# Optimization experiments

Hardware: AMD Instinct MI355X
Metric: run time of the kernel (lower is better)

Reference implementation:

```python
import jax, jax.numpy as jnp
import numpy as np

D_IN = 1024
D_OUT = 1024
N_HEADS = 16
HEAD_DIM = D_IN // N_HEADS      # 64
HEAD_DIM_V = D_OUT // N_HEADS   # 64


def setup_inputs() -> dict:
    key = jax.random.key(0)
    ks = jax.random.split(key, 7)
    s = 0.02
    x = jax.random.normal(ks[0], (4, 2048, D_IN), dtype=jnp.float32)
    Wq = jax.random.normal(ks[1], (D_IN, D_IN), dtype=jnp.float32) * s
    bq = jnp.zeros((D_IN,), dtype=jnp.float32)
    Wk = jax.random.normal(ks[2], (D_IN, D_IN), dtype=jnp.float32) * s
    bk = jnp.zeros((D_IN,), dtype=jnp.float32)
    Wv = jax.random.normal(ks[3], (D_IN, D_OUT), dtype=jnp.float32) * s
    bv = jnp.zeros((D_OUT,), dtype=jnp.float32)
    return {"x": x, "Wq": Wq, "bq": bq, "Wk": Wk, "bk": bk, "Wv": Wv, "bv": bv}


def reference(x, Wq, bq, Wk, bk, Wv, bv):
    B, S, _ = x.shape
    scale = jnp.sqrt(jnp.asarray(HEAD_DIM, dtype=jnp.float32))
    # projections -> [B, S, H, Dh] -> [B, H, S, Dh]
    q = (x @ Wq + bq).reshape(B, S, N_HEADS, HEAD_DIM).transpose(0, 2, 1, 3)
    k = (x @ Wk + bk).reshape(B, S, N_HEADS, HEAD_DIM).transpose(0, 2, 1, 3)
    v = (x @ Wv + bv).reshape(B, S, N_HEADS, HEAD_DIM_V).transpose(0, 2, 1, 3)
    # [B, H, S, S] attention scores (naive full materialization, as in source)
    scores = jnp.einsum("bhsd,bhtd->bhst", q, k) / scale
    weights = jax.nn.softmax(scores, axis=-1)
    out = jnp.einsum("bhst,bhtd->bhsd", weights, v)
    # [B, H, S, Dv] -> [B, S, H*Dv]  (out_projection NOT applied in source forward)
    return out.transpose(0, 2, 1, 3).reshape(B, S, N_HEADS * HEAD_DIM_V)
```

## Files before the change

### kernel.cpp

```cpp
#include <hip/hip_runtime.h>

#define B_  4
#define S_  2048
#define D_  1024
#define H_  16
#define DH_ 64
#define M_  (B_ * S_)

typedef __attribute__((ext_vector_type(8))) short short8;
typedef __attribute__((ext_vector_type(4))) float floatx4;

__device__ __forceinline__ float bf2f(unsigned short u) {
    union { unsigned int i; float f; } v; v.i = ((unsigned int)u) << 16; return v.f;
}
__device__ __forceinline__ unsigned short f2bf(float f) {
    union { float f; unsigned int i; } v; v.f = f;
    unsigned int r = v.i + 0x7fffu + ((v.i >> 16) & 1u);
    return (unsigned short)(r >> 16);
}
__device__ __forceinline__ unsigned int pk_trunc(float a, float b) {
    return (__float_as_uint(a) >> 16) | (__float_as_uint(b) & 0xffff0000u);
}

typedef const __attribute__((address_space(1))) unsigned int* gas_ptr;
typedef __attribute__((address_space(3))) unsigned int* las_ptr;
__device__ __forceinline__ void async_cp16(const void* g, void* l) {
    __builtin_amdgcn_global_load_lds((gas_ptr)g, (las_ptr)l, 16, 0, 0);
}

__global__ __launch_bounds__(256) void cast_x_kernel(
    const float* __restrict__ x, unsigned short* __restrict__ Ax)
{
    int i4 = blockIdx.x * 256 + threadIdx.x;
    float4 v = reinterpret_cast<const float4*>(x)[i4];
    ushort4 o;
    o.x = f2bf(v.x); o.y = f2bf(v.y); o.z = f2bf(v.z); o.w = f2bf(v.w);
    reinterpret_cast<ushort4*>(Ax)[i4] = o;
}

__global__ __launch_bounds__(256) void cast_w_T_kernel(
    const float* __restrict__ W, unsigned short* __restrict__ Wt)
{
    __shared__ unsigned short T[64][72];
    const int t = threadIdx.x;
    const int k0 = blockIdx.x * 64, n0 = blockIdx.y * 64;

    #pragma unroll
    for (int p = 0; p < 4; ++p) {
        int kr = p * 16 + (t >> 4);
        int nc = (t & 15) * 4;
        float4 v = *reinterpret_cast<const float4*>(W + (size_t)(k0 + kr) * D_ + n0 + nc);
        T[nc + 0][kr] = f2bf(v.x);
        T[nc + 1][kr] = f2bf(v.y);
        T[nc + 2][kr] = f2bf(v.z);
        T[nc + 3][kr] = f2bf(v.w);
    }
    __syncthreads();

    const int nl = t >> 2, kc = (t & 3) * 16;
    size_t base = (size_t)(n0 + nl) * D_ + k0 + kc;
    *reinterpret_cast<short8*>(Wt + base)     = *reinterpret_cast<const short8*>(&T[nl][kc]);
    *reinterpret_cast<short8*>(Wt + base + 8) = *reinterpret_cast<const short8*>(&T[nl][kc + 8]);
}

__global__ __launch_bounds__(256) void gemm_qkv_mfma(
    const unsigned short* __restrict__ Ax,
    const unsigned short* __restrict__ Wtq,
    const unsigned short* __restrict__ Wtk,
    const unsigned short* __restrict__ Wtv,
    const float* __restrict__ bq, const float* __restrict__ bk,
    const float* __restrict__ bv,
    unsigned short* __restrict__ Q, unsigned short* __restrict__ K,
    unsigned short* __restrict__ Vtg)
{
    __shared__ unsigned short As[128 * 32];
    __shared__ unsigned short Bs[128 * 32];

    const int tid = threadIdx.x;
    const int lane = tid & 63;
    const int w = tid >> 6;
    const int wm = (w >> 1) * 64, wn = (w & 1) * 64;
    const int l15 = lane & 15, quad = lane >> 4;

    const int hw   = blockIdx.x;
    const int xcd  = hw & 7;
    const int slot = hw >> 3;
    const int gcol = slot >> 3;
    const int mi   = slot & 7;
    const int m0   = (xcd * 8 + mi) * 128;
    const int n0   = (gcol & 7) * 128;
    const int mat  = gcol >> 3;

    const unsigned short* Wt = mat == 0 ? Wtq : (mat == 1 ? Wtk : Wtv);
    const float* bias        = mat == 0 ? bq  : (mat == 1 ? bk  : bv);

    const int arow = tid >> 2;
    const int acol = (tid & 3) * 8;

    floatx4 acc[4][4] = {};

    for (int kb = 0; kb < 32; ++kb) {
        int cb = kb * 32;
        __syncthreads();
        async_cp16(Ax + (size_t)(m0 + arow) * D_ + cb + acol,      As + arow * 32 + acol);
        async_cp16(Ax + (size_t)(m0 + 64 + arow) * D_ + cb + acol, As + (64 + arow) * 32 + acol);
        async_cp16(Wt + (size_t)(n0 + arow) * D_ + cb + acol,      Bs + arow * 32 + acol);
        async_cp16(Wt + (size_t)(n0 + 64 + arow) * D_ + cb + acol, Bs + (64 + arow) * 32 + acol);
        __syncthreads();

        short8 af[4], bf[4];
        #pragma unroll
        for (int i = 0; i < 4; ++i)
            af[i] = *reinterpret_cast<const short8*>(As + (wm + i * 16 + l15) * 32 + quad * 8);
        #pragma unroll
        for (int j = 0; j < 4; ++j)
            bf[j] = *reinterpret_cast<const short8*>(Bs + (wn + j * 16 + l15) * 32 + quad * 8);
        #pragma unroll
        for (int i = 0; i < 4; ++i)
            #pragma unroll
            for (int j = 0; j < 4; ++j)
                acc[i][j] = __builtin_amdgcn_mfma_f32_16x16x32_bf16(af[i], bf[j], acc[i][j], 0, 0, 0);
    }

    float bb[4];
    #pragma unroll
    for (int j = 0; j < 4; ++j) bb[j] = bias[n0 + wn + j * 16 + l15];

    if (mat == 2) {
        const int b = m0 >> 11;
        #pragma unroll
        for (int i = 0; i < 4; ++i) {
            int srow = (m0 & 2047) + wm + i * 16 + quad * 4;
            #pragma unroll
            for (int j = 0; j < 4; ++j) {
                int col = n0 + wn + j * 16 + l15;
                ushort4 o;
                o.x = f2bf(acc[i][j][0] + bb[j]);
                o.y = f2bf(acc[i][j][1] + bb[j]);
                o.z = f2bf(acc[i][j][2] + bb[j]);
                o.w = f2bf(acc[i][j][3] + bb[j]);
                *reinterpret_cast<ushort4*>(Vtg + (size_t)(b * 1024 + col) * S_ + srow) = o;
            }
        }
    } else {
        unsigned short* C = (mat == 0) ? Q : K;
        const float sc = (mat == 0) ? 0.125f : 1.0f;
        #pragma unroll
        for (int i = 0; i < 4; ++i)
            #pragma unroll
            for (int r = 0; r < 4; ++r) {
                int row = m0 + wm + i * 16 + quad * 4 + r;
                #pragma unroll
                for (int j = 0; j < 4; ++j)
                    C[(size_t)row * D_ + n0 + wn + j * 16 + l15] = f2bf((acc[i][j][r] + bb[j]) * sc);
            }
    }
}

#define KT_   64
#define PITCH 72

__global__ __launch_bounds__(256, 4) void attn_mfma(
    const unsigned short* __restrict__ Qg,
    const unsigned short* __restrict__ Kg,
    const unsigned short* __restrict__ Vtg,
    float* __restrict__ out)
{
    __shared__ unsigned short Ks[KT_ * PITCH];
    __shared__ unsigned short Vt[DH_ * PITCH];

    const int tid  = threadIdx.x;
    const int wq   = tid >> 6;
    const int lane = tid & 63;
    const int l15  = lane & 15;
    const int quad = lane >> 4;

    const int id  = blockIdx.x;
    const int bh  = (id & 7) * 8 + ((id >> 3) & 7);
    const int qt  = id >> 6;
    const int b   = bh >> 4;
    const int colbase = (bh & 15) * DH_;
    const int rowQ0 = b * S_ + qt * 128;

    short8 qf[2][2];
    #pragma unroll
    for (int g = 0; g < 2; ++g) {
        int qrow = rowQ0 + wq * 32 + g * 16 + l15;
        qf[g][0] = *reinterpret_cast<const short8*>(Qg + (size_t)qrow * D_ + colbase + quad * 8);
        qf[g][1] = *reinterpret_cast<const short8*>(Qg + (size_t)qrow * D_ + colbase + 32 + quad * 8);
    }

    floatx4 Oacc[2][4] = {};
    float lsum[2] = {0.f, 0.f};

    const int srow = tid >> 3;
    const int sc8  = (tid & 7) * 8;
    const int vc  = sc8 >> 4;
    const int vqk = (sc8 >> 2) & 3;
    const int vk0 = ((vc & 1) << 2) + ((vc >> 1) << 5) + (vqk << 3);

    const unsigned short* Kbase = Kg + (size_t)(b * S_) * D_ + colbase;
    const unsigned short* Vbase = Vtg + (size_t)(bh * 64) * S_;

    short8 kpre[2], vpre[2];
    #pragma unroll
    for (int p = 0; p < 2; ++p) {
        kpre[p] = *reinterpret_cast<const short8*>(Kbase + (size_t)(p * 32 + srow) * D_ + sc8);
        vpre[p] = *reinterpret_cast<const short8*>(Vbase + (size_t)(p * 32 + srow) * S_ + sc8);
    }

    for (int kt = 0; kt < S_ / KT_; ++kt) {
        __syncthreads();
        #pragma unroll
        for (int p = 0; p < 2; ++p) {
            *reinterpret_cast<short8*>(&Ks[(p * 32 + srow) * PITCH + sc8]) = kpre[p];
            uint4 u = __builtin_bit_cast(uint4, vpre[p]);
            uint2 lo, hi;
            lo.x = u.x; lo.y = u.y; hi.x = u.z; hi.y = u.w;
            *reinterpret_cast<uint2*>(&Vt[(p * 32 + srow) * PITCH + vk0])     = lo;
            *reinterpret_cast<uint2*>(&Vt[(p * 32 + srow) * PITCH + vk0 + 8]) = hi;
        }
        if (kt + 1 < S_ / KT_) {
            int off = (kt + 1) * KT_;
            #pragma unroll
            for (int p = 0; p < 2; ++p) {
                kpre[p] = *reinterpret_cast<const short8*>(Kbase + (size_t)(off + p * 32 + srow) * D_ + sc8);
                vpre[p] = *reinterpret_cast<const short8*>(Vbase + (size_t)(p * 32 + srow) * S_ + off + sc8);
            }
        }
        __syncthreads();

        #pragma unroll
        for (int half = 0; half < 2; ++half) {
            floatx4 s_[2][2];
            #pragma unroll
            for (int ci = 0; ci < 2; ++ci) {
                int c = half * 2 + ci;
                short8 kf0 = *reinterpret_cast<const short8*>(&Ks[(c * 16 + l15) * PITCH + quad * 8]);
                short8 kf1 = *reinterpret_cast<const short8*>(&Ks[(c * 16 + l15) * PITCH + 32 + quad * 8]);
                #pragma unroll
                for (int g = 0; g < 2; ++g) {
                    floatx4 a = {0.f, 0.f, 0.f, 0.f};
                    a = __builtin_amdgcn_mfma_f32_16x16x32_bf16(kf0, qf[g][0], a, 0, 0, 0);
                    a = __builtin_amdgcn_mfma_f32_16x16x32_bf16(kf1, qf[g][1], a, 0, 0, 0);
                    s_[g][ci] = a;
                }
            }
            short8 pa[2];
            #pragma unroll
            for (int g = 0; g < 2; ++g) {
                float p00 = __expf(s_[g][0][0]), p01 = __expf(s_[g][0][1]);
                float p02 = __expf(s_[g][0][2]), p03 = __expf(s_[g][0][3]);
                float p10 = __expf(s_[g][1][0]), p11 = __expf(s_[g][1][1]);
                float p12 = __expf(s_[g][1][2]), p13 = __expf(s_[g][1][3]);
                lsum[g] += (p00 + p01) + (p02 + p03) + (p10 + p11) + (p12 + p13);
                uint4 pu;
                pu.x = pk_trunc(p00, p01);
                pu.y = pk_trunc(p02, p03);
                pu.z = pk_trunc(p10, p11);
                pu.w = pk_trunc(p12, p13);
                pa[g] = __builtin_bit_cast(short8, pu);
            }
            #pragma unroll
            for (int d = 0; d < 4; ++d) {
                short8 vf = *reinterpret_cast<const short8*>(
                    &Vt[(d * 16 + l15) * PITCH + half * 32 + quad * 8]);
                #pragma unroll
                for (int g = 0; g < 2; ++g)
                    Oacc[g][d] = __builtin_amdgcn_mfma_f32_16x16x32_bf16(pa[g], vf, Oacc[g][d], 0, 0, 0);
            }
        }
    }

    #pragma unroll
    for (int g = 0; g < 2; ++g) {
        float lred = lsum[g];
        lred += __shfl_xor(lred, 16);
        lred += __shfl_xor(lred, 32);
        float inv[4];
        #pragma unroll
        for (int r = 0; r < 4; ++r)
            inv[r] = 1.f / __shfl(lred, quad * 4 + r);
        int orow = rowQ0 + wq * 32 + g * 16 + quad * 4;
        #pragma unroll
        for (int r = 0; r < 4; ++r)
            #pragma unroll
            for (int d = 0; d < 4; ++d)
                out[(size_t)(orow + r) * D_ + colbase + d * 16 + l15] = Oacc[g][d][r] * inv[r];
    }
}

extern "C" void kernel_launch(void* const* d_in, const int* in_sizes, int n_in,
                              void* d_out, int out_size, void* d_ws, size_t ws_size,
                              hipStream_t stream) {
    const float* x  = (const float*)d_in[0];
    const float* Wq = (const float*)d_in[1];
    const float* bq = (const float*)d_in[2];
    const float* Wk = (const float*)d_in[3];
    const float* bk = (const float*)d_in[4];
    const float* Wv = (const float*)d_in[5];
    const float* bv = (const float*)d_in[6];
    float* out = (float*)d_out;

    unsigned short* Q   = (unsigned short*)d_ws;
    unsigned short* K   = Q + (size_t)M_ * D_;
    unsigned short* Vtg = K + (size_t)M_ * D_;
    unsigned short* Ax  = Vtg + (size_t)M_ * D_;
    unsigned short* Wtq = Ax + (size_t)M_ * D_;
    unsigned short* Wtk = Wtq + (size_t)D_ * D_;
    unsigned short* Wtv = Wtk + (size_t)D_ * D_;

    cast_x_kernel<<<M_ * D_ / 4 / 256, 256, 0, stream>>>(x, Ax);
    dim3 gw(16, 16);
    cast_w_T_kernel<<<gw, 256, 0, stream>>>(Wq, Wtq);
    cast_w_T_kernel<<<gw, 256, 0, stream>>>(Wk, Wtk);
    cast_w_T_kernel<<<gw, 256, 0, stream>>>(Wv, Wtv);

    gemm_qkv_mfma<<<1536, 256, 0, stream>>>(Ax, Wtq, Wtk, Wtv, bq, bk, bv, Q, K, Vtg);

    attn_mfma<<<1024, 256, 0, stream>>>(Q, K, Vtg, out);
}
```

Measured before the change: 257.8 us.

## Use exp2 softmax with folded log2e, MFMA row sums, deeper GEMM K tile, merged weight casts

Folds log2(e) into the Q scale so softmax uses the native exp2 instruction. It also computes row sums with an MFMA against a ones vector instead of VALU adds and shuffles, and uses a perm instruction for bf16 packing. The QKV GEMM now stages 64-wide K tiles to halve barrier count, and the three weight cast launches merge into one. This trades more LDS per block and extra MFMA work for fewer VALU ops and fewer syncs and launches.

Result: faster. 246.0 us (-4.6%).

```diff
diff --git a/kernel.cpp b/kernel.cpp
--- a/kernel.cpp
+++ b/kernel.cpp
@@ -19,8 +19,18 @@
     return (unsigned short)(r >> 16);
 }
 __device__ __forceinline__ unsigned int pk_trunc(float a, float b) {
+#if __has_builtin(__builtin_amdgcn_perm)
+    return __builtin_amdgcn_perm(__float_as_uint(b), __float_as_uint(a), 0x07060302u);
+#else
     return (__float_as_uint(a) >> 16) | (__float_as_uint(b) & 0xffff0000u);
-}
+#endif
+}
+
+#if __has_builtin(__builtin_amdgcn_exp2f)
+#define EXP2(x) __builtin_amdgcn_exp2f(x)
+#else
+#define EXP2(x) __expf(0.6931471805599453f * (x))
+#endif
 
 typedef const __attribute__((address_space(1))) unsigned int* gas_ptr;
 typedef __attribute__((address_space(3))) unsigned int* las_ptr;
@@ -39,8 +49,14 @@
 }
 
 __global__ __launch_bounds__(256) void cast_w_T_kernel(
-    const float* __restrict__ W, unsigned short* __restrict__ Wt)
+    const float* __restrict__ W0, const float* __restrict__ W1,
+    const float* __restrict__ W2,
+    unsigned short* __restrict__ T0, unsigned short* __restrict__ T1,
+    unsigned short* __restrict__ T2)
 {
+    const float* W = blockIdx.z == 0 ? W0 : (blockIdx.z == 1 ? W1 : W2);
+    unsigned short* Wt = blockIdx.z == 0 ? T0 : (blockIdx.z == 1 ? T1 : T2);
+
     __shared__ unsigned short T[64][72];
     const int t = threadIdx.x;
     const int k0 = blockIdx.x * 64, n0 = blockIdx.y * 64;
@@ -73,8 +89,8 @@
     unsigned short* __restrict__ Q, unsigned short* __restrict__ K,
     unsigned short* __restrict__ Vtg)
 {
-    __shared__ unsigned short As[128 * 32];
-    __shared__ unsigned short Bs[128 * 32];
+    __shared__ unsigned short As[128 * 64];
+    __shared__ unsigned short Bs[128 * 64];
 
     const int tid = threadIdx.x;
     const int lane = tid & 63;
@@ -94,32 +110,38 @@
     const unsigned short* Wt = mat == 0 ? Wtq : (mat == 1 ? Wtk : Wtv);
     const float* bias        = mat == 0 ? bq  : (mat == 1 ? bk  : bv);
 
-    const int arow = tid >> 2;
-    const int acol = (tid & 3) * 8;
+    const int arow = tid >> 3;
+    const int acol = (tid & 7) * 8;
 
     floatx4 acc[4][4] = {};
 
-    for (int kb = 0; kb < 32; ++kb) {
-        int cb = kb * 32;
+    for (int kb = 0; kb < 16; ++kb) {
+        int cb = kb * 64;
         __syncthreads();
-        async_cp16(Ax + (size_t)(m0 + arow) * D_ + cb + acol,      As + arow * 32 + acol);
-        async_cp16(Ax + (size_t)(m0 + 64 + arow) * D_ + cb + acol, As + (64 + arow) * 32 + acol);
-        async_cp16(Wt + (size_t)(n0 + arow) * D_ + cb + acol,      Bs + arow * 32 + acol);
-        async_cp16(Wt + (size_t)(n0 + 64 + arow) * D_ + cb + acol, Bs + (64 + arow) * 32 + acol);
+        #pragma unroll
+        for (int r = 0; r < 4; ++r) {
+            async_cp16(Ax + (size_t)(m0 + r * 32 + arow) * D_ + cb + acol,
+                       As + (r * 32 + arow) * 64 + acol);
+            async_cp16(Wt + (size_t)(n0 + r * 32 + arow) * D_ + cb + acol,
+                       Bs + (r * 32 + arow) * 64 + acol);
+        }
         __syncthreads();
 
-        short8 af[4], bf[4];
-        #pragma unroll
-        for (int i = 0; i < 4; ++i)
-            af[i] = *reinterpret_cast<const short8*>(As + (wm + i * 16 + l15) * 32 + quad * 8);
-        #pragma unroll
-        for (int j = 0; j < 4; ++j)
-            bf[j] = *reinterpret_cast<const short8*>(Bs + (wn + j * 16 + l15) * 32 + quad * 8);
-        #pragma unroll
-        for (int i = 0; i < 4; ++i)
+        #pragma unroll
+        for (int kk = 0; kk < 2; ++kk) {
+            short8 af[4], bf[4];
+            #pragma unroll
+            for (int i = 0; i < 4; ++i)
+                af[i] = *reinterpret_cast<const short8*>(As + (wm + i * 16 + l15) * 64 + kk * 32 + quad * 8);
             #pragma unroll
             for (int j = 0; j < 4; ++j)
-                acc[i][j] = __builtin_amdgcn_mfma_f32_16x16x32_bf16(af[i], bf[j], acc[i][j], 0, 0, 0);
+                bf[j] = *reinterpret_cast<const short8*>(Bs + (wn + j * 16 + l15) * 64 + kk * 32 + quad * 8);
+            #pragma unroll
+            for (int i = 0; i < 4; ++i)
+                #pragma unroll
+                for (int j = 0; j < 4; ++j)
+                    acc[i][j] = __builtin_amdgcn_mfma_f32_16x16x32_bf16(af[i], bf[j], acc[i][j], 0, 0, 0);
+        }
     }
 
     float bb[4];
@@ -144,7 +166,7 @@
         }
     } else {
         unsigned short* C = (mat == 0) ? Q : K;
-        const float sc = (mat == 0) ? 0.125f : 1.0f;
+        const float sc = (mat == 0) ? 0.18033688011112042f : 1.0f;
         #pragma unroll
         for (int i = 0; i < 4; ++i)
             #pragma unroll
@@ -190,8 +212,12 @@
         qf[g][1] = *reinterpret_cast<const short8*>(Qg + (size_t)qrow * D_ + colbase + 32 + quad * 8);
     }
 
+    short8 vones;
+    #pragma unroll
+    for (int i = 0; i < 8; ++i) vones[i] = (short)0x3F80;
+
     floatx4 Oacc[2][4] = {};
-    float lsum[2] = {0.f, 0.f};
+    floatx4 Lacc[2] = {};
 
     const int srow = tid >> 3;
     const int sc8  = (tid & 7) * 8;
@@ -249,11 +275,10 @@
             short8 pa[2];
             #pragma unroll
             for (int g = 0; g < 2; ++g) {
-                float p00 = __expf(s_[g][0][0]), p01 = __expf(s_[g][0][1]);
-                float p02 = __expf(s_[g][0][2]), p03 = __expf(s_[g][0][3]);
-                float p10 = __expf(s_[g][1][0]), p11 = __expf(s_[g][1][1]);
-                float p12 = __expf(s_[g][1][2]), p13 = __expf(s_[g][1][3]);
-                lsum[g] += (p00 + p01) + (p02 + p03) + (p10 + p11) + (p12 + p13);
+                float p00 = EXP2(s_[g][0][0]), p01 = EXP2(s_[g][0][1]);
+                float p02 = EXP2(s_[g][0][2]), p03 = EXP2(s_[g][0][3]);
+                float p10 = EXP2(s_[g][1][0]), p11 = EXP2(s_[g][1][1]);
+                float p12 = EXP2(s_[g][1][2]), p13 = EXP2(s_[g][1][3]);
                 uint4 pu;
                 pu.x = pk_trunc(p00, p01);
                 pu.y = pk_trunc(p02, p03);
@@ -262,6 +287,9 @@
                 pa[g] = __builtin_bit_cast(short8, pu);
             }
             #pragma unroll
+            for (int g = 0; g < 2; ++g)
+                Lacc[g] = __builtin_amdgcn_mfma_f32_16x16x32_bf16(pa[g], vones, Lacc[g], 0, 0, 0);
+            #pragma unroll
             for (int d = 0; d < 4; ++d) {
                 short8 vf = *reinterpret_cast<const short8*>(
                     &Vt[(d * 16 + l15) * PITCH + half * 32 + quad * 8]);
@@ -274,19 +302,14 @@
 
     #pragma unroll
     for (int g = 0; g < 2; ++g) {
-        float lred = lsum[g];
-        lred += __shfl_xor(lred, 16);
-        lred += __shfl_xor(lred, 32);
-        float inv[4];
-        #pragma unroll
-        for (int r = 0; r < 4; ++r)
-            inv[r] = 1.f / __shfl(lred, quad * 4 + r);
         int orow = rowQ0 + wq * 32 + g * 16 + quad * 4;
         #pragma unroll
-        for (int r = 0; r < 4; ++r)
+        for (int r = 0; r < 4; ++r) {
+            float inv = 1.f / Lacc[g][r];
             #pragma unroll
             for (int d = 0; d < 4; ++d)
-                out[(size_t)(orow + r) * D_ + colbase + d * 16 + l15] = Oacc[g][d][r] * inv[r];
+                out[(size_t)(orow + r) * D_ + colbase + d * 16 + l15] = Oacc[g][d][r] * inv;
+        }
     }
 }
 
@@ -311,10 +334,8 @@
     unsigned short* Wtv = Wtk + (size_t)D_ * D_;
 
     cast_x_kernel<<<M_ * D_ / 4 / 256, 256, 0, stream>>>(x, Ax);
-    dim3 gw(16, 16);
-    cast_w_T_kernel<<<gw, 256, 0, stream>>>(Wq, Wtq);
-    cast_w_T_kernel<<<gw, 256, 0, stream>>>(Wk, Wtk);
-    cast_w_T_kernel<<<gw, 256, 0, stream>>>(Wv, Wtv);
+    dim3 gw(16, 16, 3);
+    cast_w_T_kernel<<<gw, 256, 0, stream>>>(Wq, Wk, Wv, Wtq, Wtk, Wtv);
 
     gemm_qkv_mfma<<<1536, 256, 0, stream>>>(Ax, Wtq, Wtk, Wtv, bq, bk, bv, Q, K, Vtg);
 
```
